# Optimization experiments

Hardware: AMD Instinct MI355X
Metric: run time of the kernel (lower is better)

Reference implementation:

```python
import jax, jax.numpy as jnp
import numpy as np

N = 100_000      # nodes (single heterogeneous node type)
E = 1_600_000    # edges per relation (avg in-degree ~16)
D = 128          # in_feats
H = 128          # rep_dim
R = 3            # relations


def setup_inputs() -> dict:
    key = jax.random.key(0)
    ks = jax.random.split(key, 1 + 6 * R)
    inp = {"x": jax.random.normal(ks[0], (N, D), jnp.float32)}
    for r in range(R):
        k = ks[1 + 6 * r: 1 + 6 * (r + 1)]
        inp[f"src{r}"] = jax.random.randint(k[0], (E,), 0, N)
        inp[f"dst{r}"] = jax.random.randint(k[1], (E,), 0, N)
        inp[f"w{r}"] = jax.random.uniform(k[2], (E,), jnp.float32)
        inp[f"Wself{r}"] = jax.random.normal(k[3], (D, H), jnp.float32) * 0.05
        inp[f"Wneigh{r}"] = jax.random.normal(k[4], (D, H), jnp.float32) * 0.05
        inp[f"b{r}"] = jax.random.normal(k[5], (H,), jnp.float32) * 0.05
    return inp


def _sage_mean(x, src, dst, w, Wself, Wneigh, b):
    """DGL SAGEConv, aggregator='mean', edge_weight=w, activation=ReLU.

    h_N[v] = (sum_{e:(u->v)} w_e * x[u]) / max(in_deg(v), 1)
    out    = relu(x @ Wself + h_N @ Wneigh + b)
    """
    msg = x[src] * w[:, None]                                   # [E, D] gather
    s = jax.ops.segment_sum(msg, dst, num_segments=N)           # [N, D] scatter-add
    deg = jax.ops.segment_sum(jnp.ones_like(w), dst, num_segments=N)  # [N]
    h_neigh = s / jnp.maximum(deg, 1.0)[:, None]                # mean; 0 for isolated nodes
    return jax.nn.relu(x @ Wself + h_neigh @ Wneigh + b)


def reference(x,
              src0, dst0, w0,
              src1, dst1, w1,
              src2, dst2, w2,
              Wself0, Wneigh0, b0,
              Wself1, Wneigh1, b1,
              Wself2, Wneigh2, b2):
    # HeteroGraphConv(aggregate='mean'): average the per-relation SAGEConv outputs.
    o0 = _sage_mean(x, src0, dst0, w0, Wself0, Wneigh0, b0)
    o1 = _sage_mean(x, src1, dst1, w1, Wself1, Wneigh1, b1)
    o2 = _sage_mean(x, src2, dst2, w2, Wself2, Wneigh2, b2)
    return (o0 + o1 + o2) / 3.0
```

## Files before the change

kernel.cpp:

```cpp
#include <hip/hip_runtime.h>
#include <hip/hip_bf16.h>
#include <cstdio>
#include <cstdint>
#include <cstddef>

#define NN 100000
#define EE 1600000
#define DD 128

#define BKT 196
#define RSHIFT 9
#define RANGE 512
#define CAP 9500
#define EPB 2048
#define ABLK ((EE + EPB - 1) / EPB)

typedef __attribute__((ext_vector_type(8))) short short8;
typedef __attribute__((ext_vector_type(4))) float floatx4;

__device__ __forceinline__ float bf2f(unsigned short u) {
    union { unsigned int u; float f; } c;
    c.u = ((unsigned int)u) << 16;
    return c.f;
}
__device__ __forceinline__ float hi2f(unsigned int p) {
    union { unsigned int u; float f; } c;
    c.u = p & 0xffff0000u;
    return c.f;
}
__device__ __forceinline__ float lo2f(unsigned int p) {
    union { unsigned int u; float f; } c;
    c.u = p << 16;
    return c.f;
}
__device__ __forceinline__ unsigned short f2bf(float f) {
    union { float f; unsigned int u; } c;
    c.f = f;
    unsigned int lsb = (c.u >> 16) & 1u;
    c.u += 0x7fffu + lsb;
    return (unsigned short)(c.u >> 16);
}

__global__ void detect_kernel(const void* x, const void* w, const void* Wm,
                              const void* b, int* flags) {
    __shared__ int ok_s;
    int bid = blockIdx.x, tid = threadIdx.x;
    if (tid == 0) ok_s = 0;
    __syncthreads();
    const unsigned short* p;
    int n;
    if (bid == 0)      { p = (const unsigned short*)x;  n = 1024; }
    else if (bid == 1) { p = (const unsigned short*)w;  n = 1024; }
    else if (bid == 2) { p = (const unsigned short*)Wm; n = 1024; }
    else               { p = (const unsigned short*)b;  n = 128;  }
    int ok = 0;
    for (int i = tid; i < n; i += blockDim.x) {
        unsigned short u = p[i];
        int e = (u >> 7) & 0xff;
        if (u == 0 || u == 0x8000 || (e >= 90 && e <= 127)) ok++;
    }
    atomicAdd(&ok_s, ok);
    __syncthreads();
    if (tid == 0) flags[bid] = (ok_s * 4 >= n * 3) ? 1 : 0;
}

__global__ void conv_x_kernel(const void* src, unsigned short* dst, int n4,
                              const int* flag) {
    if (*flag) return;
    int i = blockIdx.x * blockDim.x + threadIdx.x;
    if (i >= n4) return;
    float4 f = ((const float4*)src)[i];
    uint2 o;
    o.x = (unsigned int)f2bf(f.x) | ((unsigned int)f2bf(f.y) << 16);
    o.y = (unsigned int)f2bf(f.z) | ((unsigned int)f2bf(f.w) << 16);
    ((uint2*)dst)[i] = o;
}

__global__ void conv_f32_kernel(const void* src, float* dst, int n,
                                const int* flag) {
    int i = blockIdx.x * blockDim.x + threadIdx.x;
    if (i >= n) return;
    if (*flag) dst[i] = bf2f(((const unsigned short*)src)[i]);
    else       dst[i] = ((const float*)src)[i];
}

__global__ void conv_transposeW_kernel(const void* W, unsigned short* wT,
                                       const int* flag) {
    int i = blockIdx.x * blockDim.x + threadIdx.x;
    int d = i >> 7, h = i & 127;
    unsigned short v;
    if (*flag) v = ((const unsigned short*)W)[i];
    else       v = f2bf(((const float*)W)[i]);
    wT[h * DD + d] = v;
}

__global__ void __launch_bounds__(256) countA_kernel(
    const int* __restrict__ dstp, int* __restrict__ cnts) {
    __shared__ int hist[BKT];
    const int tid = threadIdx.x;
    const int base = blockIdx.x * EPB;
    for (int i = tid; i < BKT; i += 256) hist[i] = 0;
    __syncthreads();
#pragma unroll
    for (int k = 0; k < 8; k++) {
        int i = base + k * 256 + tid;
        if (i < EE) atomicAdd(&hist[dstp[i] >> RSHIFT], 1);
    }
    __syncthreads();
    for (int i = tid; i < BKT; i += 256)
        cnts[(size_t)blockIdx.x * BKT + i] = hist[i];
}

__global__ void __launch_bounds__(256) scanA_kernel(
    const int* __restrict__ cnts, int* __restrict__ bases,
    int* __restrict__ gcur) {
    __shared__ int s[256];
    const int b = blockIdx.x, tid = threadIdx.x;
    const int per = (ABLK + 255) / 256;
    int v[4];
    int sum = 0;
#pragma unroll
    for (int k = 0; k < 4; k++) {
        int idx = tid * per + k;
        v[k] = (idx < ABLK) ? cnts[(size_t)idx * BKT + b] : 0;
        sum += v[k];
    }
    s[tid] = sum;
    __syncthreads();
    for (int o = 1; o < 256; o <<= 1) {
        int t = (tid >= o) ? s[tid - o] : 0;
        __syncthreads();
        s[tid] += t;
        __syncthreads();
    }
    int running = s[tid] - sum;
#pragma unroll
    for (int k = 0; k < 4; k++) {
        int idx = tid * per + k;
        if (idx < ABLK) bases[(size_t)idx * BKT + b] = running;
        running += v[k];
    }
    if (tid == 255) gcur[b] = s[255];
}

__global__ void __launch_bounds__(256) placeA_kernel(
    const int* __restrict__ srcp, const int* __restrict__ dstp,
    const void* __restrict__ wp, const int* __restrict__ bases,
    int2* __restrict__ ebin, const int* __restrict__ wflag) {
    __shared__ int hist[BKT];
    __shared__ int off[BKT];
    __shared__ int cur[BKT];
    __shared__ int gbase[BKT];
    __shared__ int scan[256];
    __shared__ int2 sorted[EPB];
    __shared__ unsigned char slotb[EPB];
    const int tid = threadIdx.x;
    const int base = blockIdx.x * EPB;
    for (int i = tid; i < BKT; i += 256) hist[i] = 0;
    __syncthreads();
    int myd[8];
#pragma unroll
    for (int k = 0; k < 8; k++) {
        int i = base + k * 256 + tid;
        int d = (i < EE) ? dstp[i] : -1;
        myd[k] = d;
        if (d >= 0) atomicAdd(&hist[d >> RSHIFT], 1);
    }
    __syncthreads();
    int hv = (tid < BKT) ? hist[tid] : 0;
    scan[tid] = hv;
    __syncthreads();
    for (int o = 1; o < 256; o <<= 1) {
        int v = (tid >= o) ? scan[tid - o] : 0;
        __syncthreads();
        scan[tid] += v;
        __syncthreads();
    }
    if (tid < BKT) {
        off[tid] = scan[tid] - hv;
        cur[tid] = scan[tid] - hv;
        gbase[tid] = bases[(size_t)blockIdx.x * BKT + tid];
    }
    __syncthreads();
    const bool wbf = (*wflag != 0);
#pragma unroll
    for (int k = 0; k < 8; k++) {
        int d = myd[k];
        if (d < 0) continue;
        int i = base + k * 256 + tid;
        int b = d >> RSHIFT;
        int dloc = d - (b << RSHIFT);
        int s = srcp[i];
        float wv = wbf ? bf2f(((const unsigned short*)wp)[i])
                       : ((const float*)wp)[i];
        union { float f; int i; } c; c.f = wv;
        int pos = atomicAdd(&cur[b], 1);
        sorted[pos] = make_int2(s | (dloc << 17), c.i);
        slotb[pos] = (unsigned char)b;
    }
    __syncthreads();
    const int total = min(EPB, EE - base);
    for (int i = tid; i < total; i += 256) {
        int b = slotb[i];
        int g = gbase[b] + (i - off[b]);
        if (g < CAP) ebin[(size_t)b * CAP + g] = sorted[i];
    }
}

__global__ void __launch_bounds__(256) bucketsort_kernel(
    const int2* __restrict__ ebin, const int* __restrict__ gcur,
    int2* __restrict__ es2, int2* __restrict__ ptrv) {
    __shared__ int hc[RANGE];
    __shared__ int off[RANGE];
    __shared__ int scan[256];
    const int b = blockIdx.x, tid = threadIdx.x;
    const int base = b * CAP;
    const int cnt = min(gcur[b], CAP);
    for (int i = tid; i < RANGE; i += 256) hc[i] = 0;
    __syncthreads();
    for (int i = tid; i < cnt; i += 256) {
        int dl = ebin[base + i].x >> 17;
        atomicAdd(&hc[dl], 1);
    }
    __syncthreads();
    int a0 = hc[2 * tid], a1 = hc[2 * tid + 1];
    scan[tid] = a0 + a1;
    __syncthreads();
    for (int o = 1; o < 256; o <<= 1) {
        int v = (tid >= o) ? scan[tid - o] : 0;
        __syncthreads();
        scan[tid] += v;
        __syncthreads();
    }
    int ex = scan[tid] - (a0 + a1);
    off[2 * tid] = ex;
    off[2 * tid + 1] = ex + a0;
    ptrv[b * RANGE + 2 * tid]     = make_int2(base + ex, a0);
    ptrv[b * RANGE + 2 * tid + 1] = make_int2(base + ex + a0, a1);
    __syncthreads();
    hc[2 * tid] = off[2 * tid];
    hc[2 * tid + 1] = off[2 * tid + 1];
    __syncthreads();
    for (int i = tid; i < cnt; i += 256) {
        int2 rec = ebin[base + i];
        int dl = rec.x >> 17;
        int p = atomicAdd(&hc[dl], 1);
        es2[base + p] = make_int2(rec.x & 0x1FFFF, rec.y);
    }
}

__global__ void __launch_bounds__(256) aggregate_kernel(
    const int2* __restrict__ es, const int2* __restrict__ ptrv,
    const unsigned short* __restrict__ xc, const void* __restrict__ xraw,
    const int* __restrict__ xflag, unsigned short* __restrict__ hout) {
    int wave = (blockIdx.x * blockDim.x + threadIdx.x) >> 6;
    int lane = threadIdx.x & 63;
    if (wave >= NN) return;
    const unsigned int* x32 = (*xflag) ? (const unsigned int*)xraw
                                       : (const unsigned int*)xc;
    int2 pc = ptrv[wave];
    int beg = pc.x, deg = pc.y, end = beg + deg;
    float a0 = 0.f, a1 = 0.f;
    int e = beg;
    for (; e + 8 <= end; e += 8) {
        int2 r0 = es[e],     r1 = es[e + 1], r2 = es[e + 2], r3 = es[e + 3];
        int2 r4 = es[e + 4], r5 = es[e + 5], r6 = es[e + 6], r7 = es[e + 7];
        unsigned int p0 = x32[(size_t)r0.x * 64 + lane];
        unsigned int p1 = x32[(size_t)r1.x * 64 + lane];
        unsigned int p2 = x32[(size_t)r2.x * 64 + lane];
        unsigned int p3 = x32[(size_t)r3.x * 64 + lane];
        unsigned int p4 = x32[(size_t)r4.x * 64 + lane];
        unsigned int p5 = x32[(size_t)r5.x * 64 + lane];
        unsigned int p6 = x32[(size_t)r6.x * 64 + lane];
        unsigned int p7 = x32[(size_t)r7.x * 64 + lane];
        union { int i; float f; } c0, c1, c2, c3, c4, c5, c6, c7;
        c0.i = r0.y; c1.i = r1.y; c2.i = r2.y; c3.i = r3.y;
        c4.i = r4.y; c5.i = r5.y; c6.i = r6.y; c7.i = r7.y;
        a0 += c0.f * lo2f(p0); a1 += c0.f * hi2f(p0);
        a0 += c1.f * lo2f(p1); a1 += c1.f * hi2f(p1);
        a0 += c2.f * lo2f(p2); a1 += c2.f * hi2f(p2);
        a0 += c3.f * lo2f(p3); a1 += c3.f * hi2f(p3);
        a0 += c4.f * lo2f(p4); a1 += c4.f * hi2f(p4);
        a0 += c5.f * lo2f(p5); a1 += c5.f * hi2f(p5);
        a0 += c6.f * lo2f(p6); a1 += c6.f * hi2f(p6);
        a0 += c7.f * lo2f(p7); a1 += c7.f * hi2f(p7);
    }
    for (; e + 2 <= end; e += 2) {
        int2 r0 = es[e], r1 = es[e + 1];
        unsigned int p0 = x32[(size_t)r0.x * 64 + lane];
        unsigned int p1 = x32[(size_t)r1.x * 64 + lane];
        union { int i; float f; } c0, c1;
        c0.i = r0.y; c1.i = r1.y;
        a0 += c0.f * lo2f(p0); a1 += c0.f * hi2f(p0);
        a0 += c1.f * lo2f(p1); a1 += c1.f * hi2f(p1);
    }
    if (e < end) {
        int2 r0 = es[e];
        unsigned int p0 = x32[(size_t)r0.x * 64 + lane];
        union { int i; float f; } c0; c0.i = r0.y;
        a0 += c0.f * lo2f(p0); a1 += c0.f * hi2f(p0);
    }
    float inv = 1.0f / (float)(deg > 1 ? deg : 1);
    unsigned int outv = ((unsigned int)f2bf(a1 * inv) << 16) | f2bf(a0 * inv);
    ((unsigned int*)hout)[(size_t)wave * 64 + lane] = outv;
}

__global__ void __launch_bounds__(256) output_kernel(
    const unsigned short* __restrict__ xc, const void* __restrict__ xraw,
    const unsigned short* __restrict__ h, const unsigned short* __restrict__ wT,
    const float* __restrict__ bc, void* out, const int* __restrict__ flag) {
    __shared__ unsigned short lds[DD * 136];
    const int tid = threadIdx.x;
    const int wv = tid >> 6, lane = tid & 63;
    const int tile = blockIdx.x * 4 + wv;
    const bool active = tile < (NN / 16);
    const int c = lane & 15, q = lane >> 4;
    const int nodeRow = tile * 16 + c;
    const int xbf = *flag;
    const unsigned short* xs = xbf ? (const unsigned short*)xraw : xc;

    short8 xfrag[4];
    if (active) {
#pragma unroll
        for (int kc = 0; kc < 4; kc++)
            xfrag[kc] = *(const short8*)(xs + (size_t)nodeRow * DD + kc * 32 +
                                         q * 8);
    }

    floatx4 outacc[8];
#pragma unroll
    for (int i = 0; i < 8; i++) outacc[i] = (floatx4){0.f, 0.f, 0.f, 0.f};

    for (int r = 0; r < 3; r++) {
        floatx4 acc[8];
#pragma unroll
        for (int i = 0; i < 8; i++) acc[i] = (floatx4){0.f, 0.f, 0.f, 0.f};
        for (int p = 0; p < 2; p++) {
            const unsigned short* Wg = wT + (size_t)(r * 2 + p) * DD * DD;
            __syncthreads();
            for (int chunk = tid; chunk < DD * DD / 8; chunk += 256) {
                int row = chunk >> 4, col8 = chunk & 15;
                short8 v = *(const short8*)(Wg + row * DD + col8 * 8);
                *(short8*)(&lds[row * 136 + col8 * 8]) = v;
            }
            __syncthreads();
            if (active) {
#pragma unroll
                for (int kc = 0; kc < 4; kc++) {
                    short8 afrag;
                    if (p == 0) {
                        afrag = xfrag[kc];
                    } else {
                        afrag = *(const short8*)(h + (size_t)r * NN * DD +
                                                 (size_t)nodeRow * DD +
                                                 kc * 32 + q * 8);
                    }
#pragma unroll
                    for (int nt = 0; nt < 8; nt++) {
                        short8 bfrag = *(const short8*)(
                            &lds[(nt * 16 + c) * 136 + kc * 32 + q * 8]);
                        acc[nt] = __builtin_amdgcn_mfma_f32_16x16x32_bf16(
                            afrag, bfrag, acc[nt], 0, 0, 0);
                    }
                }
            }
        }
        if (active) {
#pragma unroll
            for (int nt = 0; nt < 8; nt++) {
                float bv = bc[r * DD + nt * 16 + c];
#pragma unroll
                for (int i = 0; i < 4; i++) {
                    float v = acc[nt][i] + bv;
                    outacc[nt][i] += fmaxf(v, 0.f);
                }
            }
        }
    }
    if (active) {
        const float sc = 1.f / 3.f;
        if (xbf) {
            unsigned short* o = (unsigned short*)out;
#pragma unroll
            for (int nt = 0; nt < 8; nt++)
#pragma unroll
                for (int i = 0; i < 4; i++)
                    o[(size_t)(tile * 16 + q * 4 + i) * DD + nt * 16 + c] =
                        f2bf(outacc[nt][i] * sc);
        } else {
            float* o = (float*)out;
#pragma unroll
            for (int nt = 0; nt < 8; nt++)
#pragma unroll
                for (int i = 0; i < 4; i++)
                    o[(size_t)(tile * 16 + q * 4 + i) * DD + nt * 16 + c] =
                        outacc[nt][i] * sc;
        }
    }
}

extern "C" void kernel_launch(void* const* d_in, const int* in_sizes, int n_in,
                              void* d_out, int out_size, void* d_ws,
                              size_t ws_size, hipStream_t stream) {
    char* w = (char*)d_ws;
    size_t off = 0;
    auto alloc = [&](size_t bytes) {
        size_t o = off;
        off = (off + bytes + 255) & ~(size_t)255;
        return o;
    };
    size_t o_flags = alloc(4 * sizeof(int));
    size_t o_gcur  = alloc(BKT * sizeof(int));
    size_t o_bc    = alloc(3 * DD * sizeof(float));
    size_t o_wT    = alloc(6 * DD * DD * sizeof(unsigned short));
    size_t o_xc    = alloc((size_t)NN * DD * sizeof(unsigned short));
    size_t o_cnts  = alloc((size_t)ABLK * BKT * sizeof(int));
    size_t o_bases = alloc((size_t)ABLK * BKT * sizeof(int));
    size_t o_ebin  = alloc((size_t)BKT * CAP * sizeof(int2));
    size_t o_es2   = alloc((size_t)BKT * CAP * sizeof(int2));
    size_t o_ptrv  = alloc((size_t)BKT * RANGE * sizeof(int2));
    size_t o_h     = alloc((size_t)3 * NN * DD * sizeof(unsigned short));
    if (ws_size < off) {
        fprintf(stderr, "kernel_launch: ws_size=%zu < needed=%zu\n", ws_size,
                off);
        return;
    }
    int* flags          = (int*)(w + o_flags);
    int* gcur           = (int*)(w + o_gcur);
    float* bc           = (float*)(w + o_bc);
    unsigned short* wT  = (unsigned short*)(w + o_wT);
    unsigned short* xc  = (unsigned short*)(w + o_xc);
    int* cnts           = (int*)(w + o_cnts);
    int* bases          = (int*)(w + o_bases);
    int2* ebin          = (int2*)(w + o_ebin);
    int2* es2           = (int2*)(w + o_es2);
    int2* ptrv          = (int2*)(w + o_ptrv);
    unsigned short* hh  = (unsigned short*)(w + o_h);

    const void* x_in = d_in[0];

    detect_kernel<<<4, 256, 0, stream>>>(x_in, d_in[3], d_in[4], d_in[6],
                                         flags);
    conv_x_kernel<<<(NN * DD / 4 + 255) / 256, 256, 0, stream>>>(
        x_in, xc, NN * DD / 4, flags + 0);
    for (int r = 0; r < 3; r++) {
        int base = 1 + 6 * r;
        conv_transposeW_kernel<<<64, 256, 0, stream>>>(
            d_in[base + 3], wT + (size_t)(r * 2 + 0) * DD * DD, flags + 2);
        conv_transposeW_kernel<<<64, 256, 0, stream>>>(
            d_in[base + 4], wT + (size_t)(r * 2 + 1) * DD * DD, flags + 2);
        conv_f32_kernel<<<1, 128, 0, stream>>>(d_in[base + 5], bc + r * DD, DD,
                                               flags + 3);
    }

    for (int r = 0; r < 3; r++) {
        int base = 1 + 6 * r;
        const int* srcp = (const int*)d_in[base + 0];
        const int* dstp = (const int*)d_in[base + 1];
        countA_kernel<<<ABLK, 256, 0, stream>>>(dstp, cnts);
        scanA_kernel<<<BKT, 256, 0, stream>>>(cnts, bases, gcur);
        placeA_kernel<<<ABLK, 256, 0, stream>>>(srcp, dstp, d_in[base + 2],
                                                bases, ebin, flags + 1);
        bucketsort_kernel<<<BKT, 256, 0, stream>>>(ebin, gcur, es2, ptrv);
        aggregate_kernel<<<(NN + 3) / 4, 256, 0, stream>>>(
            es2, ptrv, xc, x_in, flags + 0, hh + (size_t)r * NN * DD);
    }

    const int NTILES = NN / 16;
    output_kernel<<<(NTILES + 3) / 4, 256, 0, stream>>>(
        xc, x_in, hh, wT, bc, d_out, flags + 0);
}
```

Measured before the change: 578.2 us.

## Pre-swizzle weights into MFMA fragments and retile output GEMM to 128-row blocks

Weights are now pre-arranged by a small kernel into per-lane MFMA B-fragment order, so the output kernel copies both relation matrices into LDS with flat vector loads and reads fragments without padding arithmetic. Each output block now covers 128 nodes with a 2x2 wave layout of 64x64 subtiles instead of 64 nodes, so every LDS weight load is reused across four times as many rows. The output kernel also drops the per-matrix LDS reload and keeps a 4x4 accumulator grid, which uses more registers. Separately, the aggregation loop is unrolled to 16 edges to keep more gathers in flight, with 4-edge and single-edge tails.

```diff
diff --git a/kernel.cpp b/kernel.cpp
--- a/kernel.cpp
+++ b/kernel.cpp
@@ -84,14 +84,25 @@
     else       dst[i] = ((const float*)src)[i];
 }
 
-__global__ void conv_transposeW_kernel(const void* W, unsigned short* wT,
-                                       const int* flag) {
-    int i = blockIdx.x * blockDim.x + threadIdx.x;
-    int d = i >> 7, h = i & 127;
-    unsigned short v;
-    if (*flag) v = ((const unsigned short*)W)[i];
-    else       v = f2bf(((const float*)W)[i]);
-    wT[h * DD + d] = v;
+__global__ void wfrag_kernel(const void* W, unsigned short* out,
+                             const int* flag) {
+    int gid = blockIdx.x * blockDim.x + threadIdx.x;
+    int nt = gid >> 8;
+    int kc = (gid >> 6) & 3;
+    int lane = gid & 63;
+    int n = nt * 16 + (lane & 15);
+    int k0 = kc * 32 + (lane >> 4) * 8;
+    unsigned short v[8];
+    if (*flag) {
+        const unsigned short* Ws = (const unsigned short*)W;
+#pragma unroll
+        for (int j = 0; j < 8; j++) v[j] = Ws[(k0 + j) * DD + n];
+    } else {
+        const float* Ws = (const float*)W;
+#pragma unroll
+        for (int j = 0; j < 8; j++) v[j] = f2bf(Ws[(k0 + j) * DD + n]);
+    }
+    *(short8*)(out + (size_t)gid * 8) = *(short8*)v;
 }
 
 __global__ void __launch_bounds__(256) countA_kernel(
@@ -262,39 +273,36 @@
     int beg = pc.x, deg = pc.y, end = beg + deg;
     float a0 = 0.f, a1 = 0.f;
     int e = beg;
-    for (; e + 8 <= end; e += 8) {
-        int2 r0 = es[e],     r1 = es[e + 1], r2 = es[e + 2], r3 = es[e + 3];
-        int2 r4 = es[e + 4], r5 = es[e + 5], r6 = es[e + 6], r7 = es[e + 7];
+    for (; e + 16 <= end; e += 16) {
+        unsigned int p[16];
+        float cw[16];
+#pragma unroll
+        for (int k = 0; k < 16; k++) {
+            int2 r = es[e + k];
+            p[k] = x32[(size_t)r.x * 64 + lane];
+            union { int i; float f; } c; c.i = r.y;
+            cw[k] = c.f;
+        }
+#pragma unroll
+        for (int k = 0; k < 16; k++) {
+            a0 += cw[k] * lo2f(p[k]);
+            a1 += cw[k] * hi2f(p[k]);
+        }
+    }
+    for (; e + 4 <= end; e += 4) {
+        int2 r0 = es[e], r1 = es[e + 1], r2 = es[e + 2], r3 = es[e + 3];
         unsigned int p0 = x32[(size_t)r0.x * 64 + lane];
         unsigned int p1 = x32[(size_t)r1.x * 64 + lane];
         unsigned int p2 = x32[(size_t)r2.x * 64 + lane];
         unsigned int p3 = x32[(size_t)r3.x * 64 + lane];
-        unsigned int p4 = x32[(size_t)r4.x * 64 + lane];
-        unsigned int p5 = x32[(size_t)r5.x * 64 + lane];
-        unsigned int p6 = x32[(size_t)r6.x * 64 + lane];
-        unsigned int p7 = x32[(size_t)r7.x * 64 + lane];
-        union { int i; float f; } c0, c1, c2, c3, c4, c5, c6, c7;
+        union { int i; float f; } c0, c1, c2, c3;
         c0.i = r0.y; c1.i = r1.y; c2.i = r2.y; c3.i = r3.y;
-        c4.i = r4.y; c5.i = r5.y; c6.i = r6.y; c7.i = r7.y;
         a0 += c0.f * lo2f(p0); a1 += c0.f * hi2f(p0);
         a0 += c1.f * lo2f(p1); a1 += c1.f * hi2f(p1);
         a0 += c2.f * lo2f(p2); a1 += c2.f * hi2f(p2);
         a0 += c3.f * lo2f(p3); a1 += c3.f * hi2f(p3);
-        a0 += c4.f * lo2f(p4); a1 += c4.f * hi2f(p4);
-        a0 += c5.f * lo2f(p5); a1 += c5.f * hi2f(p5);
-        a0 += c6.f * lo2f(p6); a1 += c6.f * hi2f(p6);
-        a0 += c7.f * lo2f(p7); a1 += c7.f * hi2f(p7);
-    }
-    for (; e + 2 <= end; e += 2) {
-        int2 r0 = es[e], r1 = es[e + 1];
-        unsigned int p0 = x32[(size_t)r0.x * 64 + lane];
-        unsigned int p1 = x32[(size_t)r1.x * 64 + lane];
-        union { int i; float f; } c0, c1;
-        c0.i = r0.y; c1.i = r1.y;
-        a0 += c0.f * lo2f(p0); a1 += c0.f * hi2f(p0);
-        a0 += c1.f * lo2f(p1); a1 += c1.f * hi2f(p1);
-    }
-    if (e < end) {
+    }
+    for (; e < end; e++) {
         int2 r0 = es[e];
         unsigned int p0 = x32[(size_t)r0.x * 64 + lane];
         union { int i; float f; } c0; c0.i = r0.y;
@@ -305,97 +313,116 @@
     ((unsigned int*)hout)[(size_t)wave * 64 + lane] = outv;
 }
 
+#define OROWS 128
+#define OBLK ((NN + OROWS - 1) / OROWS)
+
 __global__ void __launch_bounds__(256) output_kernel(
     const unsigned short* __restrict__ xc, const void* __restrict__ xraw,
-    const unsigned short* __restrict__ h, const unsigned short* __restrict__ wT,
+    const unsigned short* __restrict__ h, const unsigned short* __restrict__ wf,
     const float* __restrict__ bc, void* out, const int* __restrict__ flag) {
-    __shared__ unsigned short lds[DD * 136];
+    __shared__ unsigned short lds[2 * DD * DD];
     const int tid = threadIdx.x;
     const int wv = tid >> 6, lane = tid & 63;
-    const int tile = blockIdx.x * 4 + wv;
-    const bool active = tile < (NN / 16);
+    const int mhalf = wv >> 1, nhalf = wv & 1;
     const int c = lane & 15, q = lane >> 4;
-    const int nodeRow = tile * 16 + c;
+    const int rowbase = blockIdx.x * OROWS + mhalf * 64;
+    const int colbase = nhalf * 64;
     const int xbf = *flag;
     const unsigned short* xs = xbf ? (const unsigned short*)xraw : xc;
 
-    short8 xfrag[4];
-    if (active) {
-#pragma unroll
-        for (int kc = 0; kc < 4; kc++)
-            xfrag[kc] = *(const short8*)(xs + (size_t)nodeRow * DD + kc * 32 +
-                                         q * 8);
-    }
-
-    floatx4 outacc[8];
-#pragma unroll
-    for (int i = 0; i < 8; i++) outacc[i] = (floatx4){0.f, 0.f, 0.f, 0.f};
+    floatx4 outacc[4][4];
+#pragma unroll
+    for (int mt = 0; mt < 4; mt++)
+#pragma unroll
+        for (int nt = 0; nt < 4; nt++)
+            outacc[mt][nt] = (floatx4){0.f, 0.f, 0.f, 0.f};
 
     for (int r = 0; r < 3; r++) {
-        floatx4 acc[8];
-#pragma unroll
-        for (int i = 0; i < 8; i++) acc[i] = (floatx4){0.f, 0.f, 0.f, 0.f};
+        __syncthreads();
+        {
+            const int4* src = (const int4*)(wf + (size_t)r * 2 * DD * DD);
+            int4* dst = (int4*)lds;
+#pragma unroll
+            for (int it = 0; it < 16; it++)
+                dst[tid + it * 256] = src[tid + it * 256];
+        }
+        __syncthreads();
+
+        floatx4 acc[4][4];
+#pragma unroll
+        for (int mt = 0; mt < 4; mt++)
+#pragma unroll
+            for (int nt = 0; nt < 4; nt++)
+                acc[mt][nt] = (floatx4){0.f, 0.f, 0.f, 0.f};
+
         for (int p = 0; p < 2; p++) {
-            const unsigned short* Wg = wT + (size_t)(r * 2 + p) * DD * DD;
-            __syncthreads();
-            for (int chunk = tid; chunk < DD * DD / 8; chunk += 256) {
-                int row = chunk >> 4, col8 = chunk & 15;
-                short8 v = *(const short8*)(Wg + row * DD + col8 * 8);
-                *(short8*)(&lds[row * 136 + col8 * 8]) = v;
+            const unsigned short* Ag =
+                (p == 0) ? xs : (h + (size_t)r * NN * DD);
+            const unsigned short* lbase = lds + (size_t)p * DD * DD;
+#pragma unroll
+            for (int kc = 0; kc < 4; kc++) {
+                short8 afrag[4];
+#pragma unroll
+                for (int mt = 0; mt < 4; mt++) {
+                    int row = rowbase + mt * 16 + c;
+                    if (row >= NN) row = NN - 1;
+                    afrag[mt] = *(const short8*)(Ag + (size_t)row * DD +
+                                                 kc * 32 + q * 8);
+                }
+                short8 bfrag[4];
+#pragma unroll
+                for (int nt = 0; nt < 4; nt++) {
+                    int fidx = ((nhalf * 4 + nt) * 4 + kc) * 64 + lane;
+                    bfrag[nt] = *(const short8*)(lbase + (size_t)fidx * 8);
+                }
+#pragma unroll
+                for (int mt = 0; mt < 4; mt++)
+#pragma unroll
+                    for (int nt = 0; nt < 4; nt++)
+                        acc[mt][nt] = __builtin_amdgcn_mfma_f32_16x16x32_bf16(
+                            afrag[mt], bfrag[nt], acc[mt][nt], 0, 0, 0);
             }
-            __syncthreads();
-            if (active) {
-#pragma unroll
-                for (int kc = 0; kc < 4; kc++) {
-                    short8 afrag;
-                    if (p == 0) {
-                        afrag = xfrag[kc];
-                    } else {
-                        afrag = *(const short8*)(h + (size_t)r * NN * DD +
-                                                 (size_t)nodeRow * DD +
-                                                 kc * 32 + q * 8);
-                    }
-#pragma unroll
-                    for (int nt = 0; nt < 8; nt++) {
-                        short8 bfrag = *(const short8*)(
-                            &lds[(nt * 16 + c) * 136 + kc * 32 + q * 8]);
-                        acc[nt] = __builtin_amdgcn_mfma_f32_16x16x32_bf16(
-                            afrag, bfrag, acc[nt], 0, 0, 0);
-                    }
+        }
+#pragma unroll
+        for (int nt = 0; nt < 4; nt++) {
+            float bv = bc[r * DD + colbase + nt * 16 + c];
+#pragma unroll
+            for (int mt = 0; mt < 4; mt++)
+#pragma unroll
+                for (int i = 0; i < 4; i++)
+                    outacc[mt][nt][i] += fmaxf(acc[mt][nt][i] + bv, 0.f);
+        }
+    }
+
+    const float sc = 1.f / 3.f;
+    if (xbf) {
+        unsigned short* o = (unsigned short*)out;
+#pragma unroll
+        for (int mt = 0; mt < 4; mt++)
+#pragma unroll
+            for (int i = 0; i < 4; i++) {
+                int row = rowbase + mt * 16 + q * 4 + i;
+                if (row < NN) {
+#pragma unroll
+                    for (int nt = 0; nt < 4; nt++)
+                        o[(size_t)row * DD + colbase + nt * 16 + c] =
+                            f2bf(outacc[mt][nt][i] * sc);
                 }
             }
-        }
-        if (active) {
-#pragma unroll
-            for (int nt = 0; nt < 8; nt++) {
-                float bv = bc[r * DD + nt * 16 + c];
-#pragma unroll
-                for (int i = 0; i < 4; i++) {
-                    float v = acc[nt][i] + bv;
-                    outacc[nt][i] += fmaxf(v, 0.f);
+    } else {
+        float* o = (float*)out;
+#pragma unroll
+        for (int mt = 0; mt < 4; mt++)
+#pragma unroll
+            for (int i = 0; i < 4; i++) {
+                int row = rowbase + mt * 16 + q * 4 + i;
+                if (row < NN) {
+#pragma unroll
+                    for (int nt = 0; nt < 4; nt++)
+                        o[(size_t)row * DD + colbase + nt * 16 + c] =
+                            outacc[mt][nt][i] * sc;
                 }
             }
-        }
-    }
-    if (active) {
-        const float sc = 1.f / 3.f;
-        if (xbf) {
-            unsigned short* o = (unsigned short*)out;
-#pragma unroll
-            for (int nt = 0; nt < 8; nt++)
-#pragma unroll
-                for (int i = 0; i < 4; i++)
-                    o[(size_t)(tile * 16 + q * 4 + i) * DD + nt * 16 + c] =
-                        f2bf(outacc[nt][i] * sc);
-        } else {
-            float* o = (float*)out;
-#pragma unroll
-            for (int nt = 0; nt < 8; nt++)
-#pragma unroll
-                for (int i = 0; i < 4; i++)
-                    o[(size_t)(tile * 16 + q * 4 + i) * DD + nt * 16 + c] =
-                        outacc[nt][i] * sc;
-        }
     }
 }
 
@@ -412,7 +439,7 @@
     size_t o_flags = alloc(4 * sizeof(int));
     size_t o_gcur  = alloc(BKT * sizeof(int));
     size_t o_bc    = alloc(3 * DD * sizeof(float));
-    size_t o_wT    = alloc(6 * DD * DD * sizeof(unsigned short));
+    size_t o_wf    = alloc(6 * DD * DD * sizeof(unsigned short));
     size_t o_xc    = alloc((size_t)NN * DD * sizeof(unsigned short));
     size_t o_cnts  = alloc((size_t)ABLK * BKT * sizeof(int));
     size_t o_bases = alloc((size_t)ABLK * BKT * sizeof(int));
@@ -428,7 +455,7 @@
     int* flags          = (int*)(w + o_flags);
     int* gcur           = (int*)(w + o_gcur);
     float* bc           = (float*)(w + o_bc);
-    unsigned short* wT  = (unsigned short*)(w + o_wT);
+    unsigned short* wf  = (unsigned short*)(w + o_wf);
     unsigned short* xc  = (unsigned short*)(w + o_xc);
     int* cnts           = (int*)(w + o_cnts);
     int* bases          = (int*)(w + o_bases);
@@ -445,10 +472,10 @@
         x_in, xc, NN * DD / 4, flags + 0);
     for (int r = 0; r < 3; r++) {
         int base = 1 + 6 * r;
-        conv_transposeW_kernel<<<64, 256, 0, stream>>>(
-            d_in[base + 3], wT + (size_t)(r * 2 + 0) * DD * DD, flags + 2);
-        conv_transposeW_kernel<<<64, 256, 0, stream>>>(
-            d_in[base + 4], wT + (size_t)(r * 2 + 1) * DD * DD, flags + 2);
+        wfrag_kernel<<<8, 256, 0, stream>>>(
+            d_in[base + 3], wf + (size_t)(r * 2 + 0) * DD * DD, flags + 2);
+        wfrag_kernel<<<8, 256, 0, stream>>>(
+            d_in[base + 4], wf + (size_t)(r * 2 + 1) * DD * DD, flags + 2);
         conv_f32_kernel<<<1, 128, 0, stream>>>(d_in[base + 5], bc + r * DD, DD,
                                                flags + 3);
     }
@@ -466,7 +493,6 @@
             es2, ptrv, xc, x_in, flags + 0, hh + (size_t)r * NN * DD);
     }
 
-    const int NTILES = NN / 16;
-    output_kernel<<<(NTILES + 3) / 4, 256, 0, stream>>>(
-        xc, x_in, hh, wT, bc, d_out, flags + 0);
-}
+    output_kernel<<<OBLK, 256, 0, stream>>>(xc, x_in, hh, wf, bc, d_out,
+                                            flags + 0);
+}
```

Measured after the change: 591.9 us. 1.02x slower.

## Batch relations into fewer launches, prepack MFMA weight fragments, widen aggregate unroll

Applied to the files above, without the earlier changes.

Merges the per-relation count, scan and aggregate kernels into single launches over all three relations, with per-relation workspace for counts, bases, sorted edges and node pointers. The weight transpose and bias conversion become one fragment-packing kernel and one bias kernel. The packed weights are laid out in MFMA B-fragment order, so the output kernel copies them into LDS with a straight vector copy instead of a padded-row layout. The aggregate loop gathers 16 edges per iteration to keep more loads in flight. These changes cut launch count and tail inefficiency at the cost of more workspace and higher register pressure in the aggregate kernel.

```diff
diff --git a/kernel.cpp b/kernel.cpp
--- a/kernel.cpp
+++ b/kernel.cpp
@@ -76,29 +76,52 @@
     ((uint2*)dst)[i] = o;
 }
 
-__global__ void conv_f32_kernel(const void* src, float* dst, int n,
-                                const int* flag) {
-    int i = blockIdx.x * blockDim.x + threadIdx.x;
-    if (i >= n) return;
-    if (*flag) dst[i] = bf2f(((const unsigned short*)src)[i]);
-    else       dst[i] = ((const float*)src)[i];
-}
-
-__global__ void conv_transposeW_kernel(const void* W, unsigned short* wT,
-                                       const int* flag) {
-    int i = blockIdx.x * blockDim.x + threadIdx.x;
-    int d = i >> 7, h = i & 127;
-    unsigned short v;
-    if (*flag) v = ((const unsigned short*)W)[i];
-    else       v = f2bf(((const float*)W)[i]);
-    wT[h * DD + d] = v;
+__global__ void conv_bias_kernel(const void* b0, const void* b1,
+                                 const void* b2, float* dst,
+                                 const int* flag) {
+    int r = blockIdx.x;
+    const void* src = (r == 0) ? b0 : (r == 1) ? b1 : b2;
+    int i = threadIdx.x;
+    if (i >= DD) return;
+    if (*flag) dst[r * DD + i] = bf2f(((const unsigned short*)src)[i]);
+    else       dst[r * DD + i] = ((const float*)src)[i];
+}
+
+__global__ void wfrag_kernel(const void* W0s, const void* W0n, const void* W1s,
+                             const void* W1n, const void* W2s, const void* W2n,
+                             unsigned short* out, const int* flag) {
+    int mat = blockIdx.x >> 3;
+    const void* W = (mat == 0) ? W0s : (mat == 1) ? W0n : (mat == 2) ? W1s
+                  : (mat == 3) ? W1n : (mat == 4) ? W2s : W2n;
+    int gid = (blockIdx.x & 7) * 256 + threadIdx.x;
+    int nt = gid >> 8;
+    int kc = (gid >> 6) & 3;
+    int lane = gid & 63;
+    int n = nt * 16 + (lane & 15);
+    int k0 = kc * 32 + (lane >> 4) * 8;
+    unsigned short v[8];
+    if (*flag) {
+        const unsigned short* Ws = (const unsigned short*)W;
+#pragma unroll
+        for (int j = 0; j < 8; j++) v[j] = Ws[(k0 + j) * DD + n];
+    } else {
+        const float* Ws = (const float*)W;
+#pragma unroll
+        for (int j = 0; j < 8; j++) v[j] = f2bf(Ws[(k0 + j) * DD + n]);
+    }
+    *(short8*)(out + (size_t)mat * DD * DD + (size_t)gid * 8) = *(short8*)v;
 }
 
 __global__ void __launch_bounds__(256) countA_kernel(
-    const int* __restrict__ dstp, int* __restrict__ cnts) {
+    const int* __restrict__ d0, const int* __restrict__ d1,
+    const int* __restrict__ d2, int* __restrict__ cnts) {
     __shared__ int hist[BKT];
+    const int rel = blockIdx.x / ABLK;
+    const int blk = blockIdx.x - rel * ABLK;
+    const int* dstp = (rel == 0) ? d0 : (rel == 1) ? d1 : d2;
+    int* cn = cnts + (size_t)rel * ABLK * BKT;
     const int tid = threadIdx.x;
-    const int base = blockIdx.x * EPB;
+    const int base = blk * EPB;
     for (int i = tid; i < BKT; i += 256) hist[i] = 0;
     __syncthreads();
 #pragma unroll
@@ -108,21 +131,25 @@
     }
     __syncthreads();
     for (int i = tid; i < BKT; i += 256)
-        cnts[(size_t)blockIdx.x * BKT + i] = hist[i];
+        cn[(size_t)blk * BKT + i] = hist[i];
 }
 
 __global__ void __launch_bounds__(256) scanA_kernel(
     const int* __restrict__ cnts, int* __restrict__ bases,
     int* __restrict__ gcur) {
     __shared__ int s[256];
-    const int b = blockIdx.x, tid = threadIdx.x;
+    const int rel = blockIdx.x / BKT;
+    const int b = blockIdx.x - rel * BKT;
+    const int* cn = cnts + (size_t)rel * ABLK * BKT;
+    int* bs = bases + (size_t)rel * ABLK * BKT;
+    const int tid = threadIdx.x;
     const int per = (ABLK + 255) / 256;
     int v[4];
     int sum = 0;
 #pragma unroll
     for (int k = 0; k < 4; k++) {
         int idx = tid * per + k;
-        v[k] = (idx < ABLK) ? cnts[(size_t)idx * BKT + b] : 0;
+        v[k] = (idx < ABLK) ? cn[(size_t)idx * BKT + b] : 0;
         sum += v[k];
     }
     s[tid] = sum;
@@ -137,10 +164,10 @@
 #pragma unroll
     for (int k = 0; k < 4; k++) {
         int idx = tid * per + k;
-        if (idx < ABLK) bases[(size_t)idx * BKT + b] = running;
+        if (idx < ABLK) bs[(size_t)idx * BKT + b] = running;
         running += v[k];
     }
-    if (tid == 255) gcur[b] = s[255];
+    if (tid == 255) gcur[rel * BKT + b] = s[255];
 }
 
 __global__ void __launch_bounds__(256) placeA_kernel(
@@ -250,51 +277,51 @@
 }
 
 __global__ void __launch_bounds__(256) aggregate_kernel(
-    const int2* __restrict__ es, const int2* __restrict__ ptrv,
+    const int2* __restrict__ es2, const int2* __restrict__ ptrv,
     const unsigned short* __restrict__ xc, const void* __restrict__ xraw,
     const int* __restrict__ xflag, unsigned short* __restrict__ hout) {
-    int wave = (blockIdx.x * blockDim.x + threadIdx.x) >> 6;
+    int gw = (blockIdx.x * blockDim.x + threadIdx.x) >> 6;
     int lane = threadIdx.x & 63;
-    if (wave >= NN) return;
+    if (gw >= 3 * NN) return;
+    int rel = gw / NN;
+    int node = gw - rel * NN;
     const unsigned int* x32 = (*xflag) ? (const unsigned int*)xraw
                                        : (const unsigned int*)xc;
-    int2 pc = ptrv[wave];
+    const int2* es = es2 + (size_t)rel * BKT * CAP;
+    int2 pc = ptrv[(size_t)rel * BKT * RANGE + node];
     int beg = pc.x, deg = pc.y, end = beg + deg;
     float a0 = 0.f, a1 = 0.f;
     int e = beg;
-    for (; e + 8 <= end; e += 8) {
-        int2 r0 = es[e],     r1 = es[e + 1], r2 = es[e + 2], r3 = es[e + 3];
-        int2 r4 = es[e + 4], r5 = es[e + 5], r6 = es[e + 6], r7 = es[e + 7];
+    for (; e + 16 <= end; e += 16) {
+        unsigned int p[16];
+        float cw[16];
+#pragma unroll
+        for (int k = 0; k < 16; k++) {
+            int2 r = es[e + k];
+            p[k] = x32[(size_t)r.x * 64 + lane];
+            union { int i; float f; } c; c.i = r.y;
+            cw[k] = c.f;
+        }
+#pragma unroll
+        for (int k = 0; k < 16; k++) {
+            a0 += cw[k] * lo2f(p[k]);
+            a1 += cw[k] * hi2f(p[k]);
+        }
+    }
+    for (; e + 4 <= end; e += 4) {
+        int2 r0 = es[e], r1 = es[e + 1], r2 = es[e + 2], r3 = es[e + 3];
         unsigned int p0 = x32[(size_t)r0.x * 64 + lane];
         unsigned int p1 = x32[(size_t)r1.x * 64 + lane];
         unsigned int p2 = x32[(size_t)r2.x * 64 + lane];
         unsigned int p3 = x32[(size_t)r3.x * 64 + lane];
-        unsigned int p4 = x32[(size_t)r4.x * 64 + lane];
-        unsigned int p5 = x32[(size_t)r5.x * 64 + lane];
-        unsigned int p6 = x32[(size_t)r6.x * 64 + lane];
-        unsigned int p7 = x32[(size_t)r7.x * 64 + lane];
-        union { int i; float f; } c0, c1, c2, c3, c4, c5, c6, c7;
+        union { int i; float f; } c0, c1, c2, c3;
         c0.i = r0.y; c1.i = r1.y; c2.i = r2.y; c3.i = r3.y;
-        c4.i = r4.y; c5.i = r5.y; c6.i = r6.y; c7.i = r7.y;
         a0 += c0.f * lo2f(p0); a1 += c0.f * hi2f(p0);
         a0 += c1.f * lo2f(p1); a1 += c1.f * hi2f(p1);
         a0 += c2.f * lo2f(p2); a1 += c2.f * hi2f(p2);
         a0 += c3.f * lo2f(p3); a1 += c3.f * hi2f(p3);
-        a0 += c4.f * lo2f(p4); a1 += c4.f * hi2f(p4);
-        a0 += c5.f * lo2f(p5); a1 += c5.f * hi2f(p5);
-        a0 += c6.f * lo2f(p6); a1 += c6.f * hi2f(p6);
-        a0 += c7.f * lo2f(p7); a1 += c7.f * hi2f(p7);
-    }
-    for (; e + 2 <= end; e += 2) {
-        int2 r0 = es[e], r1 = es[e + 1];
-        unsigned int p0 = x32[(size_t)r0.x * 64 + lane];
-        unsigned int p1 = x32[(size_t)r1.x * 64 + lane];
-        union { int i; float f; } c0, c1;
-        c0.i = r0.y; c1.i = r1.y;
-        a0 += c0.f * lo2f(p0); a1 += c0.f * hi2f(p0);
-        a0 += c1.f * lo2f(p1); a1 += c1.f * hi2f(p1);
-    }
-    if (e < end) {
+    }
+    for (; e < end; e++) {
         int2 r0 = es[e];
         unsigned int p0 = x32[(size_t)r0.x * 64 + lane];
         union { int i; float f; } c0; c0.i = r0.y;
@@ -302,14 +329,14 @@
     }
     float inv = 1.0f / (float)(deg > 1 ? deg : 1);
     unsigned int outv = ((unsigned int)f2bf(a1 * inv) << 16) | f2bf(a0 * inv);
-    ((unsigned int*)hout)[(size_t)wave * 64 + lane] = outv;
+    ((unsigned int*)hout)[(size_t)gw * 64 + lane] = outv;
 }
 
 __global__ void __launch_bounds__(256) output_kernel(
     const unsigned short* __restrict__ xc, const void* __restrict__ xraw,
-    const unsigned short* __restrict__ h, const unsigned short* __restrict__ wT,
+    const unsigned short* __restrict__ h, const unsigned short* __restrict__ wf,
     const float* __restrict__ bc, void* out, const int* __restrict__ flag) {
-    __shared__ unsigned short lds[DD * 136];
+    __shared__ unsigned short lds[DD * DD];
     const int tid = threadIdx.x;
     const int wv = tid >> 6, lane = tid & 63;
     const int tile = blockIdx.x * 4 + wv;
@@ -336,12 +363,13 @@
 #pragma unroll
         for (int i = 0; i < 8; i++) acc[i] = (floatx4){0.f, 0.f, 0.f, 0.f};
         for (int p = 0; p < 2; p++) {
-            const unsigned short* Wg = wT + (size_t)(r * 2 + p) * DD * DD;
             __syncthreads();
-            for (int chunk = tid; chunk < DD * DD / 8; chunk += 256) {
-                int row = chunk >> 4, col8 = chunk & 15;
-                short8 v = *(const short8*)(Wg + row * DD + col8 * 8);
-                *(short8*)(&lds[row * 136 + col8 * 8]) = v;
+            {
+                const int4* src = (const int4*)(wf + (size_t)(r * 2 + p) * DD * DD);
+                int4* dst = (int4*)lds;
+#pragma unroll
+                for (int it = 0; it < 8; it++)
+                    dst[tid + it * 256] = src[tid + it * 256];
             }
             __syncthreads();
             if (active) {
@@ -358,7 +386,7 @@
 #pragma unroll
                     for (int nt = 0; nt < 8; nt++) {
                         short8 bfrag = *(const short8*)(
-                            &lds[(nt * 16 + c) * 136 + kc * 32 + q * 8]);
+                            &lds[((nt * 4 + kc) * 64 + lane) * 8]);
                         acc[nt] = __builtin_amdgcn_mfma_f32_16x16x32_bf16(
                             afrag, bfrag, acc[nt], 0, 0, 0);
                     }
@@ -410,15 +438,15 @@
         return o;
     };
     size_t o_flags = alloc(4 * sizeof(int));
-    size_t o_gcur  = alloc(BKT * sizeof(int));
+    size_t o_gcur  = alloc(3 * BKT * sizeof(int));
     size_t o_bc    = alloc(3 * DD * sizeof(float));
-    size_t o_wT    = alloc(6 * DD * DD * sizeof(unsigned short));
+    size_t o_wf    = alloc(6 * DD * DD * sizeof(unsigned short));
     size_t o_xc    = alloc((size_t)NN * DD * sizeof(unsigned short));
-    size_t o_cnts  = alloc((size_t)ABLK * BKT * sizeof(int));
-    size_t o_bases = alloc((size_t)ABLK * BKT * sizeof(int));
+    size_t o_cnts  = alloc((size_t)3 * ABLK * BKT * sizeof(int));
+    size_t o_bases = alloc((size_t)3 * ABLK * BKT * sizeof(int));
     size_t o_ebin  = alloc((size_t)BKT * CAP * sizeof(int2));
-    size_t o_es2   = alloc((size_t)BKT * CAP * sizeof(int2));
-    size_t o_ptrv  = alloc((size_t)BKT * RANGE * sizeof(int2));
+    size_t o_es2   = alloc((size_t)3 * BKT * CAP * sizeof(int2));
+    size_t o_ptrv  = alloc((size_t)3 * BKT * RANGE * sizeof(int2));
     size_t o_h     = alloc((size_t)3 * NN * DD * sizeof(unsigned short));
     if (ws_size < off) {
         fprintf(stderr, "kernel_launch: ws_size=%zu < needed=%zu\n", ws_size,
@@ -428,7 +456,7 @@
     int* flags          = (int*)(w + o_flags);
     int* gcur           = (int*)(w + o_gcur);
     float* bc           = (float*)(w + o_bc);
-    unsigned short* wT  = (unsigned short*)(w + o_wT);
+    unsigned short* wf  = (unsigned short*)(w + o_wf);
     unsigned short* xc  = (unsigned short*)(w + o_xc);
     int* cnts           = (int*)(w + o_cnts);
     int* bases          = (int*)(w + o_bases);
@@ -443,30 +471,29 @@
                                          flags);
     conv_x_kernel<<<(NN * DD / 4 + 255) / 256, 256, 0, stream>>>(
         x_in, xc, NN * DD / 4, flags + 0);
+    wfrag_kernel<<<48, 256, 0, stream>>>(d_in[4], d_in[5], d_in[10], d_in[11],
+                                         d_in[16], d_in[17], wf, flags + 2);
+    conv_bias_kernel<<<3, 128, 0, stream>>>(d_in[6], d_in[12], d_in[18], bc,
+                                            flags + 3);
+
+    countA_kernel<<<3 * ABLK, 256, 0, stream>>>(
+        (const int*)d_in[2], (const int*)d_in[8], (const int*)d_in[14], cnts);
+    scanA_kernel<<<3 * BKT, 256, 0, stream>>>(cnts, bases, gcur);
+
     for (int r = 0; r < 3; r++) {
         int base = 1 + 6 * r;
-        conv_transposeW_kernel<<<64, 256, 0, stream>>>(
-            d_in[base + 3], wT + (size_t)(r * 2 + 0) * DD * DD, flags + 2);
-        conv_transposeW_kernel<<<64, 256, 0, stream>>>(
-            d_in[base + 4], wT + (size_t)(r * 2 + 1) * DD * DD, flags + 2);
-        conv_f32_kernel<<<1, 128, 0, stream>>>(d_in[base + 5], bc + r * DD, DD,
-                                               flags + 3);
-    }
-
-    for (int r = 0; r < 3; r++) {
-        int base = 1 + 6 * r;
-        const int* srcp = (const int*)d_in[base + 0];
-        const int* dstp = (const int*)d_in[base + 1];
-        countA_kernel<<<ABLK, 256, 0, stream>>>(dstp, cnts);
-        scanA_kernel<<<BKT, 256, 0, stream>>>(cnts, bases, gcur);
-        placeA_kernel<<<ABLK, 256, 0, stream>>>(srcp, dstp, d_in[base + 2],
-                                                bases, ebin, flags + 1);
-        bucketsort_kernel<<<BKT, 256, 0, stream>>>(ebin, gcur, es2, ptrv);
-        aggregate_kernel<<<(NN + 3) / 4, 256, 0, stream>>>(
-            es2, ptrv, xc, x_in, flags + 0, hh + (size_t)r * NN * DD);
-    }
+        placeA_kernel<<<ABLK, 256, 0, stream>>>(
+            (const int*)d_in[base + 0], (const int*)d_in[base + 1],
+            d_in[base + 2], bases + (size_t)r * ABLK * BKT, ebin, flags + 1);
+        bucketsort_kernel<<<BKT, 256, 0, stream>>>(
+            ebin, gcur + r * BKT, es2 + (size_t)r * BKT * CAP,
+            ptrv + (size_t)r * BKT * RANGE);
+    }
+
+    aggregate_kernel<<<(3 * NN + 3) / 4, 256, 0, stream>>>(
+        es2, ptrv, xc, x_in, flags + 0, hh);
 
     const int NTILES = NN / 16;
-    output_kernel<<<(NTILES + 3) / 4, 256, 0, stream>>>(
-        xc, x_in, hh, wT, bc, d_out, flags + 0);
-}
+    output_kernel<<<(NTILES + 3) / 4, 256, 0, stream>>>(xc, x_in, hh, wf, bc,
+                                                        d_out, flags + 0);
+}
```

Result: faster. 554.8 us (-4.0%).
